# Performance work log

Hardware: AMD Instinct MI355X
Metric: run time of the kernel (lower is better)

The kernel has to match this reference:

```python
import jax, jax.numpy as jnp
import numpy as np


def gcn_conv(x, edge_index, W, b):
    """PyG GCNConv: add self-loops, symmetric deg^{-1/2} normalization,
    linear transform, then scatter-add aggregation, plus bias."""
    n = x.shape[0]
    loops = jnp.arange(n, dtype=edge_index.dtype)
    src = jnp.concatenate([edge_index[0], loops])  # [E+N]
    dst = jnp.concatenate([edge_index[1], loops])
    ones = jnp.ones(src.shape[0], dtype=x.dtype)
    deg = jax.ops.segment_sum(ones, dst, num_segments=n)  # in-degree incl. self-loop
    dinv = jax.lax.rsqrt(jnp.maximum(deg, 1e-12))
    norm = dinv[src] * dinv[dst]  # [E+N]
    h = x @ W  # transform first (out_dim <= in_dim), [N, out]
    msg = h[src] * norm[:, None]  # gather + scale
    out = jax.ops.segment_sum(msg, dst, num_segments=n)  # scatter-add
    return out + b


def setup_inputs() -> dict:
    key = jax.random.key(0)
    ks = jax.random.split(key, 8)
    N, E, D_IN, D_OUT = 100000, 6400000, 32, 4
    x = jax.random.normal(ks[0], (N, D_IN), dtype=jnp.float32)
    edge_index = jax.random.randint(ks[1], (2, E), 0, N, dtype=jnp.int64)
    s1 = 1.0 / np.sqrt(D_IN)
    s2 = 1.0 / np.sqrt(16)
    s3 = 1.0 / np.sqrt(8)
    W1 = jax.random.uniform(ks[2], (D_IN, 16), jnp.float32, -s1, s1)
    b1 = jnp.zeros((16,), jnp.float32)
    W2 = jax.random.uniform(ks[3], (16, 8), jnp.float32, -s2, s2)
    b2 = jnp.zeros((8,), jnp.float32)
    Wfc = jax.random.uniform(ks[4], (8, D_OUT), jnp.float32, -s3, s3)
    bfc = jax.random.uniform(ks[5], (D_OUT,), jnp.float32, -s3, s3)
    return {"x": x, "edge_index": edge_index, "W1": W1, "b1": b1,
            "W2": W2, "b2": b2, "Wfc": Wfc, "bfc": bfc}


def reference(x, edge_index, W1, b1, W2, b2, Wfc, bfc):
    h = jax.nn.relu(gcn_conv(x, edge_index, W1, b1))
    h = jax.nn.relu(gcn_conv(h, edge_index, W2, b2))
    return h @ Wfc + bfc
```

## Files before the change

kernel.cpp:

```cpp
#include <hip/hip_runtime.h>
#include <hip/hip_fp16.h>

#define BLK 256
#define SHIFT 8
#define BSZ 256
#define MAXB 512
#define SRCBITS 17
#define SRCMASK ((1u << SRCBITS) - 1u)
#define TILE2 16384
#define BT 1024
#define LCAP 18432


__global__ __launch_bounds__(BT) void k_binA2(const int* __restrict__ src,
                                              const int* __restrict__ dst, int E, int N,
                                              unsigned* __restrict__ binned,
                                              int* __restrict__ bofs) {
    __shared__ int cnt[MAXB];
    __shared__ int sscan[MAXB];
    __shared__ int excl[MAXB];
    __shared__ unsigned sw[TILE2];
    int t = threadIdx.x;
    if (t < MAXB) cnt[t] = 0;
    __syncthreads();
    size_t tb = (size_t)blockIdx.x * TILE2;
    unsigned wv[16];
    int rkbk[16];
#pragma unroll
    for (int q = 0; q < 4; ++q) {
        int i4 = t + q * BT;
        size_t e0 = tb + (size_t)i4 * 4;
        int4 s4, d4;
        bool vec = (e0 + 4 <= (size_t)E);
        if (vec) {
            s4 = ((const int4*)src)[tb / 4 + i4];
            d4 = ((const int4*)dst)[tb / 4 + i4];
        }
#pragma unroll
        for (int j = 0; j < 4; ++j) {
            int idx = q * 4 + j;
            rkbk[idx] = -1;
            size_t e = e0 + j;
            int d = -1, s = -1;
            if (vec) {
                d = (j == 0) ? d4.x : (j == 1) ? d4.y : (j == 2) ? d4.z : d4.w;
                s = (j == 0) ? s4.x : (j == 1) ? s4.y : (j == 2) ? s4.z : s4.w;
            } else if (e < (size_t)E) {
                d = dst[e]; s = src[e];
            }
            if ((unsigned)d < (unsigned)N && (unsigned)s < (unsigned)N) {
                int b = d >> SHIFT;
                wv[idx] = (unsigned)s | ((unsigned)(d & (BSZ - 1)) << SRCBITS);
                int r = atomicAdd(&cnt[b], 1);
                rkbk[idx] = (r << 9) | b;
            }
        }
    }
    __syncthreads();
    if (t < MAXB) sscan[t] = cnt[t];
    __syncthreads();
    for (int off = 1; off < MAXB; off <<= 1) {
        int u = 0;
        if (t < MAXB && t >= off) u = sscan[t - off];
        __syncthreads();
        if (t < MAXB) sscan[t] += u;
        __syncthreads();
    }
    if (t < MAXB) excl[t] = sscan[t] - cnt[t];
    __syncthreads();
    int total = sscan[MAXB - 1];
#pragma unroll
    for (int idx = 0; idx < 16; ++idx) {
        int rb = rkbk[idx];
        if (rb >= 0) sw[excl[rb & 511] + (rb >> 9)] = wv[idx];
    }
    __syncthreads();
    for (int p = t; p < total; p += BT) binned[tb + p] = sw[p];
    size_t bo = (size_t)blockIdx.x * (MAXB + 1);
    if (t < MAXB) bofs[bo + t] = excl[t];
    if (t == 0) bofs[bo + MAXB] = total;
}

__global__ __launch_bounds__(MAXB) void k_bsum(const int* __restrict__ bofs, int ntiles,
                                               int* __restrict__ btot) {
    int t = threadIdx.x;
    int c = 0;
    for (int tl = blockIdx.x; tl < ntiles; tl += gridDim.x) {
        size_t bo = (size_t)tl * (MAXB + 1);
        c += bofs[bo + t + 1] - bofs[bo + t];
    }
    if (c) atomicAdd(&btot[t], c);
}

__global__ __launch_bounds__(MAXB) void k_bscan(const int* __restrict__ btot,
                                                int* __restrict__ base) {
    __shared__ int s[MAXB];
    int t = threadIdx.x;
    int v = btot[t];
    s[t] = v;
    __syncthreads();
    for (int off = 1; off < MAXB; off <<= 1) {
        int u = (t >= off) ? s[t - off] : 0;
        __syncthreads();
        s[t] += u;
        __syncthreads();
    }
    base[t] = s[t] - v;
    if (t == MAXB - 1) base[MAXB] = s[t];
}


__global__ __launch_bounds__(1024) void k_buildB4(const unsigned* __restrict__ binned,
                                                  const int* __restrict__ bofs,
                                                  const int* __restrict__ baseB,
                                                  int ntiles, int N,
                                                  float* __restrict__ dinv,
                                                  int* __restrict__ rp,
                                                  unsigned* __restrict__ csr) {
    __shared__ int h[BSZ];
    __shared__ int sc[BSZ];
    __shared__ int cnt[BSZ];
    extern __shared__ unsigned lcsr[];
    int b = blockIdx.x;
    int t = threadIdx.x;
    int gb = b << SHIFT;
    if (t < BSZ) h[t] = 0;
    __syncthreads();
    int lane = t & 63, wid = t >> 6;
    int sub = lane >> 4, sl = lane & 15;
    for (int S = wid * 4 + sub; S < ntiles; S += 64) {
        size_t bo = (size_t)S * (MAXB + 1);
        int st = bofs[bo + b], en = bofs[bo + b + 1];
        size_t base = (size_t)S * TILE2;
        int k = st + sl;
        for (; k + 16 < en; k += 32) {
            unsigned v0 = binned[base + k];
            unsigned v1 = binned[base + k + 16];
            atomicAdd(&h[v0 >> SRCBITS], 1);
            atomicAdd(&h[v1 >> SRCBITS], 1);
        }
        if (k < en) atomicAdd(&h[binned[base + k] >> SRCBITS], 1);
    }
    __syncthreads();
    if (t < BSZ) sc[t] = h[t];
    __syncthreads();
    for (int off = 1; off < BSZ; off <<= 1) {
        int u = 0;
        if (t < BSZ && t >= off) u = sc[t - off];
        __syncthreads();
        if (t < BSZ) sc[t] += u;
        __syncthreads();
    }
    int bb = baseB[b];
    int total = sc[BSZ - 1];
    if (t < BSZ) {
        int v = h[t];
        int excl = sc[t] - v;
        int gnode = gb + t;
        if (gnode < N) {
            rp[gnode] = bb + excl;
            dinv[gnode] = rsqrtf((float)v + 1.0f);
        }
        if (t == BSZ - 1) {
            int endn = gb + BSZ;
            if (endn > N) endn = N;
            rp[endn] = bb + total;
        }
        cnt[t] = excl;
    }
    __syncthreads();
    bool big = (total > LCAP);
    for (int S = wid * 4 + sub; S < ntiles; S += 64) {
        size_t bo = (size_t)S * (MAXB + 1);
        int st = bofs[bo + b], en = bofs[bo + b + 1];
        size_t base = (size_t)S * TILE2;
        int k = st + sl;
        for (; k + 16 < en; k += 32) {
            unsigned v0 = binned[base + k];
            unsigned v1 = binned[base + k + 16];
            int p0 = atomicAdd(&cnt[v0 >> SRCBITS], 1);
            int p1 = atomicAdd(&cnt[v1 >> SRCBITS], 1);
            unsigned w0 = (v0 & SRCMASK) << 5;
            unsigned w1 = (v1 & SRCMASK) << 5;
            if (!big) { lcsr[p0] = w0; lcsr[p1] = w1; }
            else      { csr[bb + p0] = w0; csr[bb + p1] = w1; }
        }
        if (k < en) {
            unsigned v = binned[base + k];
            int pos = atomicAdd(&cnt[v >> SRCBITS], 1);
            unsigned w = (v & SRCMASK) << 5;
            if (!big) lcsr[pos] = w;
            else      csr[bb + pos] = w;
        }
    }
    __syncthreads();
    if (!big) {
        for (int p = t; p < total; p += 1024) csr[bb + p] = lcsr[p];
    }
}


union Pk8 { __half h[8]; uint4 u; };
union H2U { unsigned u; __half2 h; };

__global__ __launch_bounds__(BLK) void k_transform1h(const float* __restrict__ x,
                                                     const float* __restrict__ W1,
                                                     const float* __restrict__ dinv,
                                                     __half* __restrict__ g1h, int N) {
    __shared__ float sW[32 * 16];
    for (int t = threadIdx.x; t < 512; t += BLK) sW[t] = W1[t];
    __syncthreads();
    int i = blockIdx.x * BLK + threadIdx.x;
    if (i >= N) return;
    float xr[32];
    const float4* xp = (const float4*)(x + (size_t)i * 32);
#pragma unroll
    for (int q = 0; q < 8; ++q) {
        float4 v = xp[q];
        xr[4*q] = v.x; xr[4*q+1] = v.y; xr[4*q+2] = v.z; xr[4*q+3] = v.w;
    }
    float di = dinv[i];
    Pk8 p0, p1;
#pragma unroll
    for (int j = 0; j < 16; ++j) {
        float a = 0.f;
#pragma unroll
        for (int k = 0; k < 32; ++k) a += xr[k] * sW[k * 16 + j];
        if (j < 8) p0.h[j] = __float2half_rn(a * di);
        else       p1.h[j - 8] = __float2half_rn(a * di);
    }
    uint4* gp = (uint4*)(g1h + (size_t)i * 16);
    gp[0] = p0.u;
    gp[1] = p1.u;
}


__global__ __launch_bounds__(BLK) void k_agg1(const int* __restrict__ rp,
                                              const unsigned* __restrict__ csr,
                                              const __half* __restrict__ g1h,
                                              const float* __restrict__ dinv,
                                              const float* __restrict__ b1,
                                              const float* __restrict__ W2,
                                              float* __restrict__ g2, int N) {
    __shared__ float sW[16 * 8];
    __shared__ float sb[16];
    if (threadIdx.x < 128) sW[threadIdx.x] = W2[threadIdx.x];
    if (threadIdx.x < 16) sb[threadIdx.x] = b1[threadIdx.x];
    __syncthreads();
    int wid = blockIdx.x * (BLK / 32) + (threadIdx.x >> 5);
    if (wid >= N) return;
    int alane = threadIdx.x & 63;
    int lane = threadIdx.x & 31;
    int c4 = lane & 3;
    int slot = lane >> 2;
    const char* gbase = (const char*)g1h;
    int foff = c4 << 3;
    int base_ = rp[wid], end = rp[wid + 1];
    float a0 = 0.f, a1 = 0.f, a2 = 0.f, a3 = 0.f;
    int k = base_ + slot;
    for (; k + 8 < end; k += 16) {
        unsigned v0 = csr[k], v1 = csr[k + 8];
        uint2 u0 = *(const uint2*)(gbase + v0 + foff);
        uint2 u1 = *(const uint2*)(gbase + v1 + foff);
        H2U x0, x1, y0, y1;
        x0.u = u0.x; y0.u = u0.y; x1.u = u1.x; y1.u = u1.y;
        float2 f0 = __half22float2(x0.h), f1 = __half22float2(y0.h);
        float2 f2 = __half22float2(x1.h), f3 = __half22float2(y1.h);
        a0 += f0.x + f2.x; a1 += f0.y + f2.y;
        a2 += f1.x + f3.x; a3 += f1.y + f3.y;
    }
    if (k < end) {
        unsigned v0 = csr[k];
        uint2 u0 = *(const uint2*)(gbase + v0 + foff);
        H2U x0, y0;
        x0.u = u0.x; y0.u = u0.y;
        float2 f0 = __half22float2(x0.h), f1 = __half22float2(y0.h);
        a0 += f0.x; a1 += f0.y; a2 += f1.x; a3 += f1.y;
    }
#pragma unroll
    for (int m = 4; m <= 16; m <<= 1) {
        a0 += __shfl_xor(a0, m);
        a1 += __shfl_xor(a1, m);
        a2 += __shfl_xor(a2, m);
        a3 += __shfl_xor(a3, m);
    }
    float di = dinv[wid];
    uint2 su = *(const uint2*)(gbase + ((size_t)wid << 5) + foff);
    H2U sx, sy;
    sx.u = su.x; sy.u = su.y;
    float2 sf0 = __half22float2(sx.h), sf1 = __half22float2(sy.h);
    float hh[4];
    hh[0] = fmaxf((a0 + sf0.x) * di + sb[4*c4+0], 0.f);
    hh[1] = fmaxf((a1 + sf0.y) * di + sb[4*c4+1], 0.f);
    hh[2] = fmaxf((a2 + sf1.x) * di + sb[4*c4+2], 0.f);
    hh[3] = fmaxf((a3 + sf1.y) * di + sb[4*c4+3], 0.f);
    int g4 = alane & ~3;
    int o = lane & 7;
    float a = 0.f;
#pragma unroll
    for (int kk = 0; kk < 16; ++kk) {
        float hv = __shfl(hh[kk & 3], g4 + (kk >> 2));
        a += hv * sW[kk * 8 + o];
    }
    if (lane < 8) g2[(size_t)wid * 8 + lane] = a * di;
}

__global__ __launch_bounds__(BLK) void k_agg2(const int* __restrict__ rp,
                                              const unsigned* __restrict__ csr,
                                              const float* __restrict__ g2,
                                              const float* __restrict__ dinv,
                                              const float* __restrict__ b2,
                                              const float* __restrict__ Wfc,
                                              const float* __restrict__ bfc,
                                              float* __restrict__ out, int N) {
    __shared__ float sW[8 * 4];
    __shared__ float sb2[8];
    __shared__ float sbf[4];
    if (threadIdx.x < 32) sW[threadIdx.x] = Wfc[threadIdx.x];
    if (threadIdx.x < 8) sb2[threadIdx.x] = b2[threadIdx.x];
    if (threadIdx.x < 4) sbf[threadIdx.x] = bfc[threadIdx.x];
    __syncthreads();
    int wid = blockIdx.x * (BLK / 32) + (threadIdx.x >> 5);
    if (wid >= N) return;
    int alane = threadIdx.x & 63;
    int lane = threadIdx.x & 31;
    int c4 = lane & 3;
    int slot = lane >> 2;
    const char* gbase = (const char*)g2;
    int foff = c4 << 3;
    int base_ = rp[wid], end = rp[wid + 1];
    float a0 = 0.f, a1 = 0.f;
    int k = base_ + slot;
    for (; k + 8 < end; k += 16) {
        unsigned v0 = csr[k], v1 = csr[k + 8];
        float2 f0 = *(const float2*)(gbase + v0 + foff);
        float2 f1 = *(const float2*)(gbase + v1 + foff);
        a0 += f0.x + f1.x;
        a1 += f0.y + f1.y;
    }
    if (k < end) {
        unsigned v0 = csr[k];
        float2 f0 = *(const float2*)(gbase + v0 + foff);
        a0 += f0.x; a1 += f0.y;
    }
#pragma unroll
    for (int m = 4; m <= 16; m <<= 1) {
        a0 += __shfl_xor(a0, m);
        a1 += __shfl_xor(a1, m);
    }
    float di = dinv[wid];
    float2 sf = *(const float2*)(gbase + ((size_t)wid << 5) + foff);
    float hh[2];
    hh[0] = fmaxf((a0 + sf.x) * di + sb2[2*c4+0], 0.f);
    hh[1] = fmaxf((a1 + sf.y) * di + sb2[2*c4+1], 0.f);
    int g4 = alane & ~3;
    int o = lane & 3;
    float a = 0.f;
#pragma unroll
    for (int j = 0; j < 8; ++j) {
        float hv = __shfl(hh[j & 1], g4 + (j >> 1));
        a += hv * sW[j * 4 + o];
    }
    if (lane < 4) out[(size_t)wid * 4 + lane] = a + sbf[lane];
}


__global__ __launch_bounds__(BLK) void k_count(const int* __restrict__ dst, int E, int N,
                                               float* __restrict__ cnt) {
    int i = blockIdx.x * BLK + threadIdx.x;
    if (i < E) {
        int d = dst[i];
        if ((unsigned)d < (unsigned)N) atomicAdd(&cnt[d], 1.0f);
    }
}
__global__ __launch_bounds__(BLK) void k_dinv_f(float* __restrict__ cnt, int N) {
    int i = blockIdx.x * BLK + threadIdx.x;
    if (i < N) cnt[i] = rsqrtf(cnt[i] + 1.0f);
}
__global__ __launch_bounds__(BLK) void k_transform1(const float* __restrict__ x,
                                                    const float* __restrict__ W1,
                                                    const float* __restrict__ dinv,
                                                    float* __restrict__ g1, int N) {
    __shared__ float sW[32 * 16];
    for (int t = threadIdx.x; t < 512; t += BLK) sW[t] = W1[t];
    __syncthreads();
    int i = blockIdx.x * BLK + threadIdx.x;
    if (i >= N) return;
    float xr[32];
    const float4* xp = (const float4*)(x + (size_t)i * 32);
#pragma unroll
    for (int q = 0; q < 8; ++q) {
        float4 v = xp[q];
        xr[4*q] = v.x; xr[4*q+1] = v.y; xr[4*q+2] = v.z; xr[4*q+3] = v.w;
    }
    float di = dinv[i];
    float o[16];
#pragma unroll
    for (int j = 0; j < 16; ++j) {
        float a = 0.f;
#pragma unroll
        for (int k = 0; k < 32; ++k) a += xr[k] * sW[k * 16 + j];
        o[j] = a * di;
    }
    float4* gp = (float4*)(g1 + (size_t)i * 16);
#pragma unroll
    for (int q = 0; q < 4; ++q)
        gp[q] = make_float4(o[4*q], o[4*q+1], o[4*q+2], o[4*q+3]);
}
template <int F>
__global__ __launch_bounds__(BLK) void k_edge_agg(const int* __restrict__ src,
                                                  const int* __restrict__ dst,
                                                  int E, int N,
                                                  const float* __restrict__ g,
                                                  float* __restrict__ agg) {
    size_t t = (size_t)blockIdx.x * BLK + threadIdx.x;
    int e = (int)(t / F);
    int f = (int)(t & (F - 1));
    if (e >= E) return;
    int s = src[e], d = dst[e];
    if ((unsigned)s >= (unsigned)N || (unsigned)d >= (unsigned)N) return;
    atomicAdd(&agg[(size_t)d * F + f], g[(size_t)s * F + f]);
}
__global__ __launch_bounds__(BLK) void k_node1(const float* __restrict__ g1,
                                               const float* __restrict__ agg1,
                                               const float* __restrict__ dinv,
                                               const float* __restrict__ b1,
                                               const float* __restrict__ W2,
                                               float* __restrict__ g2, int N) {
    __shared__ float sW[16 * 8];
    __shared__ float sb[16];
    for (int t = threadIdx.x; t < 128; t += BLK) sW[t] = W2[t];
    if (threadIdx.x < 16) sb[threadIdx.x] = b1[threadIdx.x];
    __syncthreads();
    int i = blockIdx.x * BLK + threadIdx.x;
    if (i >= N) return;
    float di = dinv[i];
    const float4* gp = (const float4*)(g1 + (size_t)i * 16);
    const float4* ap = (const float4*)(agg1 + (size_t)i * 16);
    float h[16];
#pragma unroll
    for (int q = 0; q < 4; ++q) {
        float4 gv = gp[q], av = ap[q];
        h[4*q+0] = fmaxf((av.x + gv.x) * di + sb[4*q+0], 0.f);
        h[4*q+1] = fmaxf((av.y + gv.y) * di + sb[4*q+1], 0.f);
        h[4*q+2] = fmaxf((av.z + gv.z) * di + sb[4*q+2], 0.f);
        h[4*q+3] = fmaxf((av.w + gv.w) * di + sb[4*q+3], 0.f);
    }
    float o[8];
#pragma unroll
    for (int j = 0; j < 8; ++j) {
        float a = 0.f;
#pragma unroll
        for (int k = 0; k < 16; ++k) a += h[k] * sW[k * 8 + j];
        o[j] = a * di;
    }
    float4* op = (float4*)(g2 + (size_t)i * 8);
    op[0] = make_float4(o[0], o[1], o[2], o[3]);
    op[1] = make_float4(o[4], o[5], o[6], o[7]);
}
__global__ __launch_bounds__(BLK) void k_node2(const float* __restrict__ g2,
                                               const float* __restrict__ agg2,
                                               const float* __restrict__ dinv,
                                               const float* __restrict__ b2,
                                               const float* __restrict__ Wfc,
                                               const float* __restrict__ bfc,
                                               float* __restrict__ out, int N) {
    __shared__ float sW[8 * 4];
    __shared__ float sb2[8];
    __shared__ float sbf[4];
    if (threadIdx.x < 32) sW[threadIdx.x] = Wfc[threadIdx.x];
    if (threadIdx.x < 8) sb2[threadIdx.x] = b2[threadIdx.x];
    if (threadIdx.x < 4) sbf[threadIdx.x] = bfc[threadIdx.x];
    __syncthreads();
    int i = blockIdx.x * BLK + threadIdx.x;
    if (i >= N) return;
    float di = dinv[i];
    const float4* gp = (const float4*)(g2 + (size_t)i * 8);
    const float4* ap = (const float4*)(agg2 + (size_t)i * 8);
    float h[8];
#pragma unroll
    for (int q = 0; q < 2; ++q) {
        float4 gv = gp[q], av = ap[q];
        h[4*q+0] = fmaxf((av.x + gv.x) * di + sb2[4*q+0], 0.f);
        h[4*q+1] = fmaxf((av.y + gv.y) * di + sb2[4*q+1], 0.f);
        h[4*q+2] = fmaxf((av.z + gv.z) * di + sb2[4*q+2], 0.f);
        h[4*q+3] = fmaxf((av.w + gv.w) * di + sb2[4*q+3], 0.f);
    }
    float o[4];
#pragma unroll
    for (int k = 0; k < 4; ++k) {
        float a = sbf[k];
#pragma unroll
        for (int j = 0; j < 8; ++j) a += h[j] * sW[j * 4 + k];
        o[k] = a;
    }
    ((float4*)(out + (size_t)i * 4))[0] = make_float4(o[0], o[1], o[2], o[3]);
}


extern "C" void kernel_launch(void* const* d_in, const int* in_sizes, int n_in,
                              void* d_out, int out_size, void* d_ws, size_t ws_size,
                              hipStream_t stream) {
    const float* x   = (const float*)d_in[0];
    const int*   ei  = (const int*)d_in[1];
    const float* W1  = (const float*)d_in[2];
    const float* b1  = (const float*)d_in[3];
    const float* W2  = (const float*)d_in[4];
    const float* b2  = (const float*)d_in[5];
    const float* Wfc = (const float*)d_in[6];
    const float* bfc = (const float*)d_in[7];

    int N = in_sizes[0] / 32;
    int E = in_sizes[1] / 2;
    const int* src = ei;
    const int* dst = ei + (size_t)E;

    int ntiles = (E + TILE2 - 1) / TILE2;
    int nbuk = (N + BSZ - 1) >> SHIFT;

    size_t w_g1h  = 0;
    size_t w_g2   = w_g1h + (size_t)8 * N;
    size_t w_dinv = w_g2 + (size_t)8 * N;
    size_t w_rp   = w_dinv + (size_t)N;
    size_t w_btot = w_rp + (size_t)N + 1;
    size_t w_bs   = w_btot + MAXB;
    size_t w_bofs = w_bs + MAXB + 1;
    size_t w_bin  = (w_bofs + (size_t)ntiles * (MAXB + 1) + 3) & ~(size_t)3;
    size_t w_csr  = w_bin + (size_t)E;
    size_t need   = (w_csr + (size_t)E) * 4;

    bool fast = (ws_size >= need) && (N <= (1 << SRCBITS)) && (nbuk <= MAXB);

    if (fast) {
        float*    ws     = (float*)d_ws;
        __half*   g1h    = (__half*)(ws + w_g1h);
        float*    g2     = ws + w_g2;
        float*    dinv   = ws + w_dinv;
        int*      rp     = (int*)(ws + w_rp);
        int*      btot   = (int*)(ws + w_btot);
        int*      baseB  = (int*)(ws + w_bs);
        int*      bofs   = (int*)(ws + w_bofs);
        unsigned* binned = (unsigned*)(ws + w_bin);
        unsigned* csr    = (unsigned*)(ws + w_csr);

        int nnode = (N + BLK - 1) / BLK;
        int nagg = (N + (BLK / 32) - 1) / (BLK / 32);

        hipMemsetAsync(btot, 0, MAXB * 4, stream);

        k_binA2<<<ntiles, BT, 0, stream>>>(src, dst, E, N, binned, bofs);
        k_bsum<<<128, MAXB, 0, stream>>>(bofs, ntiles, btot);
        k_bscan<<<1, MAXB, 0, stream>>>(btot, baseB);
        k_buildB4<<<nbuk, 1024, LCAP * 4, stream>>>(binned, bofs, baseB,
                                                    ntiles, N, dinv, rp, csr);
        k_transform1h<<<nnode, BLK, 0, stream>>>(x, W1, dinv, g1h, N);
        k_agg1<<<nagg, BLK, 0, stream>>>(rp, csr, g1h, dinv, b1, W2, g2, N);
        k_agg2<<<nagg, BLK, 0, stream>>>(rp, csr, g2, dinv, b2, Wfc, bfc,
                                         (float*)d_out, N);
    } else {
        float* ws   = (float*)d_ws;
        float* dinv = ws;
        float* g1   = dinv + (size_t)N;
        float* agg1 = g1 + (size_t)16 * N;
        float* g2   = agg1 + (size_t)16 * N;
        float* agg2 = g2 + (size_t)8 * N;

        hipMemsetAsync(dinv, 0, (size_t)N * 4, stream);
        hipMemsetAsync(agg1, 0, (size_t)16 * N * 4, stream);
        hipMemsetAsync(agg2, 0, (size_t)8 * N * 4, stream);

        k_count<<<(E + BLK - 1) / BLK, BLK, 0, stream>>>(dst, E, N, dinv);
        k_dinv_f<<<(N + BLK - 1) / BLK, BLK, 0, stream>>>(dinv, N);
        k_transform1<<<(N + BLK - 1) / BLK, BLK, 0, stream>>>(x, W1, dinv, g1, N);
        {
            size_t tot = (size_t)E * 16;
            k_edge_agg<16><<<(unsigned)((tot + BLK - 1) / BLK), BLK, 0, stream>>>(src, dst, E, N, g1, agg1);
        }
        k_node1<<<(N + BLK - 1) / BLK, BLK, 0, stream>>>(g1, agg1, dinv, b1, W2, g2, N);
        {
            size_t tot = (size_t)E * 8;
            k_edge_agg<8><<<(unsigned)((tot + BLK - 1) / BLK), BLK, 0, stream>>>(src, dst, E, N, g2, agg2);
        }
        k_node2<<<(N + BLK - 1) / BLK, BLK, 0, stream>>>(g2, agg2, dinv, b2, Wfc, bfc, (float*)d_out, N);
    }
}
```

Baseline: 159.7 us.

## Halve bucket size, vectorize binned/CSR stores, nontemporal CSR loads

Bucket width drops from 256 to 128 destinations and the bucket count doubles to 1024, with the local CSR capacity shrunk to match. Smaller buckets are meant to let the per-bucket CSR build fit in shared memory more often and give more parallel blocks. The binned and CSR writeback loops now use 16-byte uint4 stores, with alignment handling added, and the aggregation kernels read CSR indices with nontemporal loads to avoid polluting cache. The trade-off is a longer scan (1024 entries) and a larger per-tile offset table in the binning kernel.

```diff
diff --git a/kernel.cpp b/kernel.cpp
--- a/kernel.cpp
+++ b/kernel.cpp
@@ -2,14 +2,14 @@
 #include <hip/hip_fp16.h>
 
 #define BLK 256
-#define SHIFT 8
-#define BSZ 256
-#define MAXB 512
+#define SHIFT 7
+#define BSZ 128
+#define MAXB 1024
 #define SRCBITS 17
 #define SRCMASK ((1u << SRCBITS) - 1u)
 #define TILE2 16384
 #define BT 1024
-#define LCAP 18432
+#define LCAP 9728
 
 
 __global__ __launch_bounds__(BT) void k_binA2(const int* __restrict__ src,
@@ -21,7 +21,7 @@
     __shared__ int excl[MAXB];
     __shared__ unsigned sw[TILE2];
     int t = threadIdx.x;
-    if (t < MAXB) cnt[t] = 0;
+    cnt[t] = 0;
     __syncthreads();
     size_t tb = (size_t)blockIdx.x * TILE2;
     unsigned wv[16];
@@ -52,32 +52,36 @@
                 int b = d >> SHIFT;
                 wv[idx] = (unsigned)s | ((unsigned)(d & (BSZ - 1)) << SRCBITS);
                 int r = atomicAdd(&cnt[b], 1);
-                rkbk[idx] = (r << 9) | b;
+                rkbk[idx] = (r << 10) | b;
             }
         }
     }
     __syncthreads();
-    if (t < MAXB) sscan[t] = cnt[t];
+    sscan[t] = cnt[t];
     __syncthreads();
     for (int off = 1; off < MAXB; off <<= 1) {
-        int u = 0;
-        if (t < MAXB && t >= off) u = sscan[t - off];
+        int u = (t >= off) ? sscan[t - off] : 0;
         __syncthreads();
-        if (t < MAXB) sscan[t] += u;
+        sscan[t] += u;
         __syncthreads();
     }
-    if (t < MAXB) excl[t] = sscan[t] - cnt[t];
+    excl[t] = sscan[t] - cnt[t];
     __syncthreads();
     int total = sscan[MAXB - 1];
 #pragma unroll
     for (int idx = 0; idx < 16; ++idx) {
         int rb = rkbk[idx];
-        if (rb >= 0) sw[excl[rb & 511] + (rb >> 9)] = wv[idx];
-    }
-    __syncthreads();
-    for (int p = t; p < total; p += BT) binned[tb + p] = sw[p];
+        if (rb >= 0) sw[excl[rb & 1023] + (rb >> 10)] = wv[idx];
+    }
+    __syncthreads();
+    int nq = total >> 2;
+    for (int p = t; p < nq; p += BT) {
+        uint4 v = *(const uint4*)&sw[p << 2];
+        *(uint4*)(binned + tb + ((size_t)p << 2)) = v;
+    }
+    for (int p = (nq << 2) + t; p < total; p += BT) binned[tb + p] = sw[p];
     size_t bo = (size_t)blockIdx.x * (MAXB + 1);
-    if (t < MAXB) bofs[bo + t] = excl[t];
+    bofs[bo + t] = excl[t];
     if (t == 0) bofs[bo + MAXB] = total;
 }
 
@@ -195,7 +199,17 @@
     }
     __syncthreads();
     if (!big) {
-        for (int p = t; p < total; p += 1024) csr[bb + p] = lcsr[p];
+        int h0 = ((bb + 3) & ~3) - bb;
+        if (h0 > total) h0 = total;
+        if (t < h0) csr[bb + t] = lcsr[t];
+        int rem = total - h0;
+        int nq = (rem > 0) ? (rem >> 2) : 0;
+        for (int p = t; p < nq; p += 1024) {
+            int lp = h0 + (p << 2);
+            uint4 v = make_uint4(lcsr[lp], lcsr[lp + 1], lcsr[lp + 2], lcsr[lp + 3]);
+            *(uint4*)(csr + bb + lp) = v;
+        }
+        for (int p = h0 + (nq << 2) + t; p < total; p += 1024) csr[bb + p] = lcsr[p];
     }
 }
 
@@ -259,7 +273,8 @@
     float a0 = 0.f, a1 = 0.f, a2 = 0.f, a3 = 0.f;
     int k = base_ + slot;
     for (; k + 8 < end; k += 16) {
-        unsigned v0 = csr[k], v1 = csr[k + 8];
+        unsigned v0 = __builtin_nontemporal_load(csr + k);
+        unsigned v1 = __builtin_nontemporal_load(csr + k + 8);
         uint2 u0 = *(const uint2*)(gbase + v0 + foff);
         uint2 u1 = *(const uint2*)(gbase + v1 + foff);
         H2U x0, x1, y0, y1;
@@ -270,7 +285,7 @@
         a2 += f1.x + f3.x; a3 += f1.y + f3.y;
     }
     if (k < end) {
-        unsigned v0 = csr[k];
+        unsigned v0 = __builtin_nontemporal_load(csr + k);
         uint2 u0 = *(const uint2*)(gbase + v0 + foff);
         H2U x0, y0;
         x0.u = u0.x; y0.u = u0.y;
@@ -332,14 +347,15 @@
     float a0 = 0.f, a1 = 0.f;
     int k = base_ + slot;
     for (; k + 8 < end; k += 16) {
-        unsigned v0 = csr[k], v1 = csr[k + 8];
+        unsigned v0 = __builtin_nontemporal_load(csr + k);
+        unsigned v1 = __builtin_nontemporal_load(csr + k + 8);
         float2 f0 = *(const float2*)(gbase + v0 + foff);
         float2 f1 = *(const float2*)(gbase + v1 + foff);
         a0 += f0.x + f1.x;
         a1 += f0.y + f1.y;
     }
     if (k < end) {
-        unsigned v0 = csr[k];
+        unsigned v0 = __builtin_nontemporal_load(csr + k);
         float2 f0 = *(const float2*)(gbase + v0 + foff);
         a0 += f0.x; a1 += f0.y;
     }
@@ -526,8 +542,8 @@
     size_t w_bs   = w_btot + MAXB;
     size_t w_bofs = w_bs + MAXB + 1;
     size_t w_bin  = (w_bofs + (size_t)ntiles * (MAXB + 1) + 3) & ~(size_t)3;
-    size_t w_csr  = w_bin + (size_t)E;
-    size_t need   = (w_csr + (size_t)E) * 4;
+    size_t w_csr  = (w_bin + (size_t)E + 3) & ~(size_t)3;
+    size_t need   = (w_csr + (size_t)E + 4) * 4;
 
     bool fast = (ws_size >= need) && (N <= (1 << SRCBITS)) && (nbuk <= MAXB);
 
```

Result: slower. 202.0 us (+26.5%).
